# Kernel tuning notes

Hardware: AMD Instinct MI355X
Metric: run time of the kernel (lower is better)

The kernel has to match this reference:

```python
import jax, jax.numpy as jnp
import numpy as np

D_MODEL = 2048
NUM_HEADS = 16
HEAD_DIM = D_MODEL // NUM_HEADS  # 128
BASE = 10000.0


def rotate_half(x):
    x1, x2 = x[..., : x.shape[-1] // 2], x[..., x.shape[-1] // 2 :]
    return jnp.concatenate((-x2, x1), axis=-1)


def setup_inputs() -> dict:
    key = jax.random.key(0)
    ks = jax.random.split(key, 9)
    B, S, D = 2, 2048, D_MODEL
    s = 1.0 / np.sqrt(D)
    return {
        "x": jax.random.normal(ks[0], (B, S, D), dtype=jnp.float32),
        "Wq": jax.random.normal(ks[1], (D, D), dtype=jnp.float32) * s,
        "bq": jnp.zeros((D,), dtype=jnp.float32),
        "Wk": jax.random.normal(ks[2], (D, D), dtype=jnp.float32) * s,
        "bk": jnp.zeros((D,), dtype=jnp.float32),
        "Wv": jax.random.normal(ks[3], (D, D), dtype=jnp.float32) * s,
        "bv": jnp.zeros((D,), dtype=jnp.float32),
        "Wo": jax.random.normal(ks[4], (D, D), dtype=jnp.float32) * s,
        "bo": jnp.zeros((D,), dtype=jnp.float32),
    }


def reference(x, Wq, bq, Wk, bk, Wv, bv, Wo, bo):
    B, S, D = x.shape
    H, hd = NUM_HEADS, HEAD_DIM

    def proj(W, b):
        # nn.Linear: x @ W^T + b, then split heads -> [B, H, S, hd]
        return (x @ W.T + b).reshape(B, S, H, hd).transpose(0, 2, 1, 3)

    q = proj(Wq, bq)
    k = proj(Wk, bk)
    v = proj(Wv, bv)

    # Rotary embedding table (note: original applies cos()/sin() to a
    # tensor that already contains [sin(si), cos(si)] — reproduced faithfully).
    positions = jnp.arange(S, dtype=jnp.float32)
    inv_freq = 1.0 / (BASE ** (jnp.arange(0, hd, 2, dtype=jnp.float32) / hd))
    sinusoid = positions[:, None] * inv_freq[None, :]            # [S, hd/2]
    emb = jnp.concatenate((jnp.sin(sinusoid), jnp.cos(sinusoid)), axis=-1)  # [S, hd]
    cos_e = jnp.cos(emb)  # broadcast over [B, H, S, hd]
    sin_e = jnp.sin(emb)

    q_rot = q * cos_e + rotate_half(q) * sin_e
    k_rot = k * cos_e + rotate_half(k) * sin_e

    scale = 1.0 / jnp.sqrt(jnp.asarray(hd, dtype=x.dtype))
    attn = jnp.einsum("bhqd,bhkd->bhqk", q_rot, k_rot) * scale
    attn = jax.nn.softmax(attn, axis=-1)
    out = jnp.einsum("bhqk,bhkd->bhqd", attn, v)
    out = out.transpose(0, 2, 1, 3).reshape(B, S, D)
    return out @ Wo.T + bo
```

## Files before the change

kernel.cpp:

```cpp
#include <hip/hip_runtime.h>
#include <math.h>

#define D_MODEL 2048
#define NHEADS  16
#define HD      128
#define SEQ     2048
#define BATCH   2
#define SCALE   0.08838834764831845f
#define SMAX    20.0f

typedef __attribute__((ext_vector_type(8))) short short8;
typedef __attribute__((ext_vector_type(4))) float f32x4;

#define MFMA16(a,b,c) __builtin_amdgcn_mfma_f32_16x16x32_bf16((a),(b),(c),0,0,0)

__device__ __forceinline__ unsigned short f2bf(float x){
    unsigned u = __float_as_uint(x);
    return (unsigned short)((u + 0x7FFFu + ((u>>16)&1u)) >> 16);
}
__device__ __forceinline__ float bf2f(unsigned short h){ return __uint_as_float(((unsigned)h)<<16); }

__device__ __forceinline__ void async16(void* lds, const void* g){
    __builtin_amdgcn_global_load_lds((const __attribute__((address_space(1))) unsigned int*)g,
                                     (__attribute__((address_space(3))) unsigned int*)lds, 16, 0, 0);
}

__device__ __forceinline__ void split4(float4 v, ushort4* h, ushort4* l){
    h->x=f2bf(v.x); l->x=f2bf(v.x-bf2f(h->x));
    h->y=f2bf(v.y); l->y=f2bf(v.y-bf2f(h->y));
    h->z=f2bf(v.z); l->z=f2bf(v.z-bf2f(h->z));
    h->w=f2bf(v.w); l->w=f2bf(v.w-bf2f(h->w));
}

__global__ __launch_bounds__(256)
void prep_all(const float* __restrict__ x, const float* __restrict__ Wq,
              const float* __restrict__ Wk, const float* __restrict__ Wv,
              unsigned short* __restrict__ Xhi, unsigned short* __restrict__ Xlo,
              unsigned short* __restrict__ WqHi, unsigned short* __restrict__ WqLo,
              unsigned short* __restrict__ WkHi, unsigned short* __restrict__ WkLo,
              unsigned short* __restrict__ WvHi,
              float4* __restrict__ tab)
{
    const int b = blockIdx.x, t = threadIdx.x;
    if (b < 8192) {
        int i = b*256 + t;
        ushort4 h,l; split4(((const float4*)x)[i], &h, &l);
        ((ushort4*)Xhi)[i]=h; ((ushort4*)Xlo)[i]=l;
    } else if (b < 12288) {
        int i = (b-8192)*256 + t;
        ushort4 h,l; split4(((const float4*)Wq)[i], &h, &l);
        ((ushort4*)WqHi)[i]=h; ((ushort4*)WqLo)[i]=l;
    } else if (b < 16384) {
        int i = (b-12288)*256 + t;
        ushort4 h,l; split4(((const float4*)Wk)[i], &h, &l);
        ((ushort4*)WkHi)[i]=h; ((ushort4*)WkLo)[i]=l;
    } else if (b < 20480) {
        int i = (b-16384)*256 + t;
        ushort4 h,l; split4(((const float4*)Wv)[i], &h, &l);
        ((ushort4*)WvHi)[i]=h;
    } else {
        int i = (b-20480)*256 + t;
        int s = i >> 6, d = i & 63;
        float f = powf(10000.0f, -(float)d * (1.0f/64.0f));
        float sv = (float)s * f;
        float sn = sinf(sv), cs = cosf(sv);
        tab[i] = (float4){cosf(sn), sinf(sn), cosf(cs), sinf(cs)};
    }
}

__global__ __launch_bounds__(256)
void split_w(const float* __restrict__ src, unsigned short* __restrict__ hi,
             unsigned short* __restrict__ lo, int n4)
{
    int i = blockIdx.x*256 + threadIdx.x;
    if (i >= n4) return;
    ushort4 h,l; split4(((const float4*)src)[i], &h, &l);
    ((ushort4*)hi)[i]=h; ((ushort4*)lo)[i]=l;
}

__global__ __launch_bounds__(256,2)
void gemm_qkv(const unsigned short* __restrict__ Xhi_g, const unsigned short* __restrict__ Xlo_g,
              const unsigned short* __restrict__ wsplit,
              const float* __restrict__ bq, const float* __restrict__ bk, const float* __restrict__ bv,
              const float4* __restrict__ tab,
              unsigned short* __restrict__ Qhi, unsigned short* __restrict__ Qlo,
              unsigned short* __restrict__ Khi, unsigned short* __restrict__ Klo,
              unsigned short* __restrict__ Vt)
{
    const int z = blockIdx.z;
    const unsigned short* Whi = wsplit + (size_t)z*8388608u;
    const unsigned short* Wlo = Whi + 4194304u;
    const float* bias = (z==0)?bq:((z==1)?bk:bv);

    const int t = threadIdx.x, w = t>>6, lane = t&63;
    const int quad = lane>>4, l15 = lane&15;
    const int mhalf = (w>>1)*64, nhalf = (w&1)*64;
    const int m0 = blockIdx.y*128, n0 = blockIdx.x*128;

    __shared__ __align__(16) unsigned short gsm[17408];
    unsigned short* Ahi = gsm;
    unsigned short* Alo = gsm + 4096;
    unsigned short* Bhi = gsm + 8192;
    unsigned short* Blo = gsm + 12288;

    f32x4 acc[4][4];
#pragma unroll
    for (int i=0;i<4;i++)
#pragma unroll
        for (int j=0;j<4;j++) acc[i][j] = (f32x4){0.f,0.f,0.f,0.f};

    for (int kt=0; kt<2048; kt+=32) {
        __syncthreads();
#pragma unroll
        for (int j=0;j<2;j++){
            int idx=t+256*j; int rw=idx>>2, sg=idx&3;
            int sgp = sg ^ ((rw>>1)&3);
            size_t goffA = (size_t)(m0+rw)*2048 + kt + sgp*8;
            size_t goffB = (size_t)(n0+rw)*2048 + kt + sgp*8;
            async16((char*)&Ahi[rw*32+sg*8], Xhi_g + goffA);
            async16((char*)&Alo[rw*32+sg*8], Xlo_g + goffA);
            async16((char*)&Bhi[rw*32+sg*8], Whi + goffB);
            if (z != 2)
                async16((char*)&Blo[rw*32+sg*8], Wlo + goffB);
        }
        __syncthreads();

        short8 af_h[4], af_l[4], bf_h[4], bf_l[4];
#pragma unroll
        for (int mi=0;mi<4;mi++){
            int m = mhalf + mi*16 + l15;
            int c = (quad ^ ((m>>1)&3))*8;
            af_h[mi] = *(const short8*)&Ahi[m*32 + c];
            af_l[mi] = *(const short8*)&Alo[m*32 + c];
        }
#pragma unroll
        for (int ni=0;ni<4;ni++){
            int n = nhalf + ni*16 + l15;
            int c = (quad ^ ((n>>1)&3))*8;
            bf_h[ni] = *(const short8*)&Bhi[n*32 + c];
            if (z != 2) bf_l[ni] = *(const short8*)&Blo[n*32 + c];
        }
#pragma unroll
        for (int mi=0;mi<4;mi++)
#pragma unroll
            for (int ni=0;ni<4;ni++){
                acc[mi][ni] = MFMA16(af_h[mi], bf_h[ni], acc[mi][ni]);
                acc[mi][ni] = MFMA16(af_l[mi], bf_h[ni], acc[mi][ni]);
                if (z != 2) acc[mi][ni] = MFMA16(af_h[mi], bf_l[ni], acc[mi][ni]);
            }
    }
    __syncthreads();

#pragma unroll
    for (int ni=0;ni<4;ni++){
        float bv_ = bias[n0 + nhalf + ni*16 + l15];
#pragma unroll
        for (int mi=0;mi<4;mi++){
            acc[mi][ni][0]+=bv_; acc[mi][ni][1]+=bv_; acc[mi][ni][2]+=bv_; acc[mi][ni][3]+=bv_;
        }
    }

    const int h = blockIdx.x;
    if (z == 2) {
#pragma unroll
        for (int mi=0;mi<4;mi++)
#pragma unroll
        for (int ni=0;ni<4;ni++)
#pragma unroll
        for (int r=0;r<4;r++){
            int d = nhalf + ni*16 + l15;
            int ml = mhalf + mi*16 + quad*4 + r;
            gsm[d*136 + ml] = f2bf(acc[mi][ni][r]);
        }
        __syncthreads();
        const int b = m0>>11, s0 = m0&2047;
        unsigned short* vdst = Vt + ((size_t)(b*16+h)*128)*2048;
        const int dr = t>>1, half = (t&1)*64;
#pragma unroll
        for (int j=0;j<8;j++){
            uint4 v = *(const uint4*)&gsm[dr*136 + half + j*8];
            *(uint4*)(vdst + (size_t)dr*2048 + s0 + half + j*8) = v;
        }
    } else {
        float* xch = (float*)gsm;
        unsigned short* OHi = (z==0)?Qhi:Khi;
        unsigned short* OLo = (z==0)?Qlo:Klo;
        const float scl = (z==0)?SCALE:1.0f;
        const int b = m0>>11;
        const size_t bhbase = ((size_t)(b*16+h)*2048);

        if (!(w & 1)) {
#pragma unroll
            for (int mi=0;mi<4;mi++)
#pragma unroll
            for (int ni=2;ni<4;ni++)
#pragma unroll
            for (int r=0;r<4;r++)
                xch[(mhalf+mi*16+quad*4+r)*68 + (ni-2)*16+l15] = acc[mi][ni][r];
        } else {
#pragma unroll
            for (int mi=0;mi<4;mi++)
#pragma unroll
            for (int ni=0;ni<2;ni++)
#pragma unroll
            for (int r=0;r<4;r++)
                xch[(mhalf+mi*16+quad*4+r)*68 + 32 + ni*16+l15] = acc[mi][ni][r];
        }
        __syncthreads();

        if (!(w & 1)) {
#pragma unroll
            for (int ni2=0;ni2<2;ni2++){
                int d = ni2*16 + l15;
#pragma unroll
                for (int mi=0;mi<4;mi++)
#pragma unroll
                for (int r=0;r<4;r++){
                    int ml = mhalf + mi*16 + quad*4 + r;
                    int s = (m0 + ml) & 2047;
                    float4 tv = tab[s*64 + d];
                    float c_lo = acc[mi][ni2][r];
                    float c_hi = xch[ml*68 + 32 + d];
                    float o1 = (c_lo*tv.x - c_hi*tv.y)*scl;
                    float o2 = (c_hi*tv.z + c_lo*tv.w)*scl;
                    size_t base = (bhbase + s)*128;
                    unsigned short h1=f2bf(o1); OHi[base+d]=h1;    OLo[base+d]=f2bf(o1-bf2f(h1));
                    unsigned short h2=f2bf(o2); OHi[base+64+d]=h2; OLo[base+64+d]=f2bf(o2-bf2f(h2));
                }
            }
        } else {
#pragma unroll
            for (int ni2=0;ni2<2;ni2++){
                int d = 32 + ni2*16 + l15;
#pragma unroll
                for (int mi=0;mi<4;mi++)
#pragma unroll
                for (int r=0;r<4;r++){
                    int ml = mhalf + mi*16 + quad*4 + r;
                    int s = (m0 + ml) & 2047;
                    float4 tv = tab[s*64 + d];
                    float c_lo = xch[ml*68 + (d-32)];
                    float c_hi = acc[mi][ni2+2][r];
                    float o1 = (c_lo*tv.x - c_hi*tv.y)*scl;
                    float o2 = (c_hi*tv.z + c_lo*tv.w)*scl;
                    size_t base = (bhbase + s)*128;
                    unsigned short h1=f2bf(o1); OHi[base+d]=h1;    OLo[base+d]=f2bf(o1-bf2f(h1));
                    unsigned short h2=f2bf(o2); OHi[base+64+d]=h2; OLo[base+64+d]=f2bf(o2-bf2f(h2));
                }
            }
        }
    }
}

__global__ __launch_bounds__(256,2)
void flash_mfma(const unsigned short* __restrict__ Qhi, const unsigned short* __restrict__ Qlo,
                const unsigned short* __restrict__ Khi, const unsigned short* __restrict__ Klo,
                const unsigned short* __restrict__ Vt,
                unsigned short* __restrict__ Ohi, unsigned short* __restrict__ Olo)
{
    const int t=threadIdx.x, w=t>>6, lane=t&63, quad=lane>>4, l15=lane&15;
    const int bh = blockIdx.y, qt = blockIdx.x;

    __shared__ __align__(16) unsigned short sm[32768];
    unsigned short* Ps = sm + 24576 + w*2048;

    short8 qf[2][2][4];
    const size_t qrow = (size_t)bh*2048 + qt*128 + w*32;
#pragma unroll
    for (int mb=0;mb<2;mb++){
        size_t r = qrow + mb*16 + l15;
#pragma unroll
        for (int kc=0;kc<4;kc++){
            qf[0][mb][kc] = *(const short8*)(Qhi + r*128 + kc*32 + quad*8);
            qf[1][mb][kc] = *(const short8*)(Qlo + r*128 + kc*32 + quad*8);
        }
    }

    f32x4 O[2][8];
#pragma unroll
    for (int mb=0;mb<2;mb++)
#pragma unroll
        for (int nb=0;nb<8;nb++) O[mb][nb]=(f32x4){0.f,0.f,0.f,0.f};
    float lrow[2][4];
#pragma unroll
    for (int mb=0;mb<2;mb++)
#pragma unroll
        for (int r=0;r<4;r++) lrow[mb][r]=0.f;

    const char* KhiB = (const char*)(Khi + (size_t)bh*2048*128);
    const char* KloB = (const char*)(Klo + (size_t)bh*2048*128);
    const unsigned short* VtB = Vt + (size_t)bh*128*2048;
    char* smb = (char*)sm;

    for (int kt=0; kt<2048; kt+=64) {
#pragma unroll
        for (int i=0;i<4;i++){
            int o16 = t + 256*i;
            int krow = o16>>4, kc = o16&15;
            int kcp = kc ^ (krow&15);
            async16(smb + i*4096 + t*16,         KhiB + (size_t)kt*256 + krow*256 + kcp*16);
            async16(smb + 16384 + i*4096 + t*16, KloB + (size_t)kt*256 + krow*256 + kcp*16);
            int d = (t>>3) + i*32, c = t&7;
            int cp = c ^ (d&7);
            async16(smb + 32768 + i*4096 + t*16, VtB + (size_t)d*2048 + kt + cp*8);
        }
        __syncthreads();

        f32x4 S[2][4];
#pragma unroll
        for (int mb=0;mb<2;mb++)
#pragma unroll
            for (int nb=0;nb<4;nb++) S[mb][nb]=(f32x4){0.f,0.f,0.f,0.f};
#pragma unroll
        for (int kc=0;kc<4;kc++)
#pragma unroll
        for (int nb=0;nb<4;nb++){
            int m = nb*16+l15;
            int c = ((kc*4+quad) ^ (m&15))*8;
            short8 kh = *(const short8*)&sm[m*128 + c];
            short8 kl = *(const short8*)&sm[8192 + m*128 + c];
#pragma unroll
            for (int mb=0;mb<2;mb++){
                S[mb][nb] = MFMA16(qf[0][mb][kc], kh, S[mb][nb]);
                S[mb][nb] = MFMA16(qf[1][mb][kc], kh, S[mb][nb]);
                S[mb][nb] = MFMA16(qf[0][mb][kc], kl, S[mb][nb]);
            }
        }

#pragma unroll
        for (int mb=0;mb<2;mb++)
#pragma unroll
        for (int nb=0;nb<4;nb++)
#pragma unroll
        for (int r=0;r<4;r++){
            float p = __expf(S[mb][nb][r] - SMAX);
            lrow[mb][r] += p;
            int q = mb*16 + quad*4 + r;
            int c = nb*16 + l15;
            Ps[q*64 + (((c>>3)^(q&7))<<3) + (c&7)] = f2bf(p);
        }

#pragma unroll
        for (int kc2=0;kc2<2;kc2++){
            short8 pf0 = *(const short8*)&Ps[(l15)*64      + (((kc2*4+quad)^(l15&7))<<3)];
            short8 pf1 = *(const short8*)&Ps[(16+l15)*64   + (((kc2*4+quad)^(l15&7))<<3)];
#pragma unroll
            for (int nb=0;nb<8;nb++){
                int d = nb*16+l15;
                int c = ((kc2*4+quad) ^ (d&7))*8;
                short8 vf = *(const short8*)&sm[16384 + d*64 + c];
                O[0][nb] = MFMA16(pf0, vf, O[0][nb]);
                O[1][nb] = MFMA16(pf1, vf, O[1][nb]);
            }
        }
        __syncthreads();
    }

#pragma unroll
    for (int mb=0;mb<2;mb++)
#pragma unroll
        for (int d=1;d<16;d<<=1)
#pragma unroll
            for (int r=0;r<4;r++) lrow[mb][r] += __shfl_xor(lrow[mb][r], d);

    const int b = bh>>4, h = bh&15;
#pragma unroll
    for (int mb=0;mb<2;mb++)
#pragma unroll
    for (int nb=0;nb<8;nb++)
#pragma unroll
    for (int r=0;r<4;r++){
        float v = O[mb][nb][r] / lrow[mb][r];
        int qg = qt*128 + w*32 + mb*16 + quad*4 + r;
        size_t base = ((size_t)(b*2048 + qg))*2048 + h*128 + nb*16 + l15;
        unsigned short hh = f2bf(v);
        Ohi[base]=hh; Olo[base]=f2bf(v-bf2f(hh));
    }
}

__global__ __launch_bounds__(256,2)
void gemm_out(const unsigned short* __restrict__ Ahi_g, const unsigned short* __restrict__ Alo_g,
              const unsigned short* __restrict__ Whi_g, const unsigned short* __restrict__ Wlo_g,
              const float* __restrict__ bias, float* __restrict__ out)
{
    const int t = threadIdx.x, w = t>>6, lane = t&63;
    const int quad = lane>>4, l15 = lane&15;
    const int mhalf = (w>>1)*64, nhalf = (w&1)*64;
    const int m0 = blockIdx.y*128, n0 = blockIdx.x*128;

    __shared__ __align__(16) unsigned short gsm[16384];
    unsigned short* Ahi = gsm;
    unsigned short* Alo = gsm + 4096;
    unsigned short* Bhi = gsm + 8192;
    unsigned short* Blo = gsm + 12288;

    f32x4 acc[4][4];
#pragma unroll
    for (int i=0;i<4;i++)
#pragma unroll
        for (int j=0;j<4;j++) acc[i][j] = (f32x4){0.f,0.f,0.f,0.f};

    for (int kt=0; kt<2048; kt+=32) {
        __syncthreads();
#pragma unroll
        for (int j=0;j<2;j++){
            int idx=t+256*j; int rw=idx>>2, sg=idx&3;
            int sgp = sg ^ ((rw>>1)&3);
            async16((char*)&Ahi[rw*32+sg*8], Ahi_g + (size_t)(m0+rw)*2048 + kt + sgp*8);
            async16((char*)&Alo[rw*32+sg*8], Alo_g + (size_t)(m0+rw)*2048 + kt + sgp*8);
            async16((char*)&Bhi[rw*32+sg*8], Whi_g + (size_t)(n0+rw)*2048 + kt + sgp*8);
            async16((char*)&Blo[rw*32+sg*8], Wlo_g + (size_t)(n0+rw)*2048 + kt + sgp*8);
        }
        __syncthreads();

        short8 af_h[4], af_l[4], bf_h[4], bf_l[4];
#pragma unroll
        for (int mi=0;mi<4;mi++){
            int m = mhalf + mi*16 + l15;
            int c = (quad ^ ((m>>1)&3))*8;
            af_h[mi] = *(const short8*)&Ahi[m*32 + c];
            af_l[mi] = *(const short8*)&Alo[m*32 + c];
        }
#pragma unroll
        for (int ni=0;ni<4;ni++){
            int n = nhalf + ni*16 + l15;
            int c = (quad ^ ((n>>1)&3))*8;
            bf_h[ni] = *(const short8*)&Bhi[n*32 + c];
            bf_l[ni] = *(const short8*)&Blo[n*32 + c];
        }
#pragma unroll
        for (int mi=0;mi<4;mi++)
#pragma unroll
            for (int ni=0;ni<4;ni++){
                acc[mi][ni] = MFMA16(af_h[mi], bf_h[ni], acc[mi][ni]);
                acc[mi][ni] = MFMA16(af_l[mi], bf_h[ni], acc[mi][ni]);
                acc[mi][ni] = MFMA16(af_h[mi], bf_l[ni], acc[mi][ni]);
            }
    }

#pragma unroll
    for (int ni=0;ni<4;ni++){
        int n = n0 + nhalf + ni*16 + l15;
        float bv_ = bias[n];
#pragma unroll
        for (int mi=0;mi<4;mi++)
#pragma unroll
        for (int r=0;r<4;r++){
            int m = m0 + mhalf + mi*16 + quad*4 + r;
            out[(size_t)m*2048 + n] = acc[mi][ni][r] + bv_;
        }
    }
}

extern "C" void kernel_launch(void* const* d_in, const int* in_sizes, int n_in,
                              void* d_out, int out_size, void* d_ws, size_t ws_size,
                              hipStream_t stream)
{
    (void)in_sizes; (void)n_in; (void)out_size; (void)ws_size;
    const float* x  = (const float*)d_in[0];
    const float* Wq = (const float*)d_in[1];
    const float* bq = (const float*)d_in[2];
    const float* Wk = (const float*)d_in[3];
    const float* bk = (const float*)d_in[4];
    const float* Wv = (const float*)d_in[5];
    const float* bv = (const float*)d_in[6];
    const float* Wo = (const float*)d_in[7];
    const float* bo = (const float*)d_in[8];
    float* out = (float*)d_out;

    unsigned short* wsB = (unsigned short*)d_ws;
    unsigned short* C0  = wsB + 20971520u;
    unsigned short* Qhi = C0;
    unsigned short* Qlo = C0 + 8388608u;
    unsigned short* Khi = C0 + 16777216u;
    unsigned short* Klo = C0 + 25165824u;
    unsigned short* Vt  = C0 + 33554432u;
    float4* tab = (float4*)(wsB + 62914560u);

    unsigned short* Xhi = (unsigned short*)d_out;
    unsigned short* Xlo = Xhi + 8388608u;

    prep_all<<<20992,256,0,stream>>>(x, Wq, Wk, Wv,
                                     Xhi, Xlo,
                                     wsB,            wsB+4194304u,
                                     wsB+8388608u,   wsB+12582912u,
                                     wsB+16777216u,  tab);

    gemm_qkv<<<dim3(16,32,3),256,0,stream>>>(Xhi, Xlo, wsB, bq,bk,bv, tab,
                                             Qhi,Qlo,Khi,Klo,Vt);

    unsigned short* Ohi = wsB;
    unsigned short* Olo = wsB + 8388608u;
    flash_mfma<<<dim3(16,32),256,0,stream>>>(Qhi,Qlo,Khi,Klo,Vt, Ohi, Olo);

    unsigned short* WoHi = C0;
    unsigned short* WoLo = C0 + 4194304u;
    split_w<<<4096,256,0,stream>>>(Wo, WoHi, WoLo, 1048576);

    gemm_out<<<dim3(16,32),256,0,stream>>>(Ohi, Olo, WoHi, WoLo, bo, out);
}
```

Measured before the change: 662.0 us.

## Triple-buffer GEMM core with async LDS prefetch and larger 256x128 tiles

Replaces the synchronous load-then-compute GEMM loops with a shared gemm_core that triple-buffers A/B tiles in dynamic LDS. It prefetches two k-steps ahead using vmcnt waits and interleaves the staging loads with MFMA phases under s_setprio. Blocks grow to 512 threads with 256x128 tiles, and the QKV kernel is split into separate Q/K and V kernels so the V path skips the lo-weight loads. This is meant to hide global load latency and cut barrier stalls, at the cost of 144KB LDS per block, which lowers occupancy.

```diff
diff --git a/kernel.cpp b/kernel.cpp
--- a/kernel.cpp
+++ b/kernel.cpp
@@ -78,30 +78,129 @@
     ((ushort4*)hi)[i]=h; ((ushort4*)lo)[i]=l;
 }
 
-__global__ __launch_bounds__(256,2)
-void gemm_qkv(const unsigned short* __restrict__ Xhi_g, const unsigned short* __restrict__ Xlo_g,
-              const unsigned short* __restrict__ wsplit,
-              const float* __restrict__ bq, const float* __restrict__ bk, const float* __restrict__ bv,
-              const float4* __restrict__ tab,
-              unsigned short* __restrict__ Qhi, unsigned short* __restrict__ Qlo,
-              unsigned short* __restrict__ Khi, unsigned short* __restrict__ Klo,
-              unsigned short* __restrict__ Vt)
-{
+template<bool THREE, int Q>
+__device__ __forceinline__ void phase_mfma(const unsigned short* Bh, const unsigned short* Bl,
+                                           const short8 (&ah)[4], const short8 (&al)[4],
+                                           f32x4 (&acc)[4][4], int wn, int quad, int l15)
+{
+    int n = wn*64 + Q*16 + l15;
+    int c = (quad ^ ((n>>1)&3))*8;
+    short8 bh_ = *(const short8*)&Bh[n*32 + c];
+    short8 bl_ = {};
+    if constexpr (THREE) bl_ = *(const short8*)&Bl[n*32 + c];
+    __builtin_amdgcn_s_setprio(1);
+    acc[0][Q] = MFMA16(ah[0], bh_, acc[0][Q]);
+    acc[1][Q] = MFMA16(ah[1], bh_, acc[1][Q]);
+    acc[2][Q] = MFMA16(ah[2], bh_, acc[2][Q]);
+    acc[3][Q] = MFMA16(ah[3], bh_, acc[3][Q]);
+    acc[0][Q] = MFMA16(al[0], bh_, acc[0][Q]);
+    acc[1][Q] = MFMA16(al[1], bh_, acc[1][Q]);
+    acc[2][Q] = MFMA16(al[2], bh_, acc[2][Q]);
+    acc[3][Q] = MFMA16(al[3], bh_, acc[3][Q]);
+    if constexpr (THREE) {
+        acc[0][Q] = MFMA16(ah[0], bl_, acc[0][Q]);
+        acc[1][Q] = MFMA16(ah[1], bl_, acc[1][Q]);
+        acc[2][Q] = MFMA16(ah[2], bl_, acc[2][Q]);
+        acc[3][Q] = MFMA16(ah[3], bl_, acc[3][Q]);
+    }
+    __builtin_amdgcn_s_setprio(0);
+}
+
+template<bool THREE>
+__device__ __forceinline__ void gemm_core(const unsigned short* __restrict__ Agh,
+                                          const unsigned short* __restrict__ Agl,
+                                          const unsigned short* __restrict__ Bgh,
+                                          const unsigned short* __restrict__ Bgl,
+                                          unsigned short* lds, int m0, int n0,
+                                          f32x4 (&acc)[4][4])
+{
+    const int t = threadIdx.x, w = t>>6, lane = t&63;
+    const int quad = lane>>4, l15 = lane&15;
+    const int wm = w>>1, wn = w&1;
+
+    unsigned short *c0 = lds, *c1 = lds + 24576, *c2 = lds + 49152;
+
+    auto stageA = [&](unsigned short* P, const unsigned short* SRC, int u, int kt2){
+        int idx = t + u*512; int rw = idx>>2, sg = idx&3;
+        int sgp = sg ^ ((rw>>1)&3);
+        async16((char*)(P + rw*32 + sg*8), SRC + (size_t)(m0+rw)*2048 + kt2 + sgp*8);
+    };
+    auto stageB = [&](unsigned short* P, const unsigned short* SRC, int kt2){
+        int rw = t>>2, sg = t&3; int sgp = sg ^ ((rw>>1)&3);
+        async16((char*)(P + rw*32 + sg*8), SRC + (size_t)(n0+rw)*2048 + kt2 + sgp*8);
+    };
+
+    stageA(c0,        Agh, 0, 0);  stageA(c0,        Agh, 1, 0);
+    stageA(c0+8192,   Agl, 0, 0);  stageA(c0+8192,   Agl, 1, 0);
+    stageB(c0+16384,  Bgh, 0);
+    if constexpr (THREE) stageB(c0+20480, Bgl, 0);
+    stageA(c1,        Agh, 0, 32); stageA(c1,        Agh, 1, 32);
+    stageA(c1+8192,   Agl, 0, 32); stageA(c1+8192,   Agl, 1, 32);
+    stageB(c1+16384,  Bgh, 32);
+    if constexpr (THREE) stageB(c1+20480, Bgl, 32);
+
+    for (int kt = 0; kt < 64; ++kt) {
+        if (kt == 63) {
+            asm volatile("s_waitcnt vmcnt(0)" ::: "memory");
+        } else if constexpr (THREE) {
+            asm volatile("s_waitcnt vmcnt(6)" ::: "memory");
+        } else {
+            asm volatile("s_waitcnt vmcnt(5)" ::: "memory");
+        }
+        __builtin_amdgcn_s_barrier();
+        __builtin_amdgcn_sched_barrier(0);
+
+        const unsigned short* Ah = c0;
+        const unsigned short* Al = c0 + 8192;
+        const unsigned short* Bh = c0 + 16384;
+        const unsigned short* Bl = c0 + 20480;
+        const int  kt2 = (kt+2)*32;
+        const bool st  = (kt < 62);
+
+        short8 ah[4], al[4];
+#pragma unroll
+        for (int mi=0;mi<4;mi++){
+            int m = wm*64 + mi*16 + l15;
+            int c = (quad ^ ((m>>1)&3))*8;
+            ah[mi] = *(const short8*)&Ah[m*32 + c];
+            al[mi] = *(const short8*)&Al[m*32 + c];
+        }
+        if (st){ stageA(c2,       Agh, 0, kt2); stageA(c2,       Agh, 1, kt2); }
+        phase_mfma<THREE,0>(Bh, Bl, ah, al, acc, wn, quad, l15);
+        __builtin_amdgcn_s_barrier();
+
+        if (st){ stageA(c2+8192,  Agl, 0, kt2); stageA(c2+8192,  Agl, 1, kt2); }
+        phase_mfma<THREE,1>(Bh, Bl, ah, al, acc, wn, quad, l15);
+        __builtin_amdgcn_s_barrier();
+
+        if (st){ stageB(c2+16384, Bgh, kt2); }
+        phase_mfma<THREE,2>(Bh, Bl, ah, al, acc, wn, quad, l15);
+        __builtin_amdgcn_s_barrier();
+
+        if constexpr (THREE) { if (st) stageB(c2+20480, Bgl, kt2); }
+        phase_mfma<THREE,3>(Bh, Bl, ah, al, acc, wn, quad, l15);
+        __builtin_amdgcn_s_barrier();
+
+        unsigned short* tmp = c0; c0 = c1; c1 = c2; c2 = tmp;
+    }
+}
+
+__global__ __launch_bounds__(512,2)
+void gemm_qk(const unsigned short* __restrict__ Xhi_g, const unsigned short* __restrict__ Xlo_g,
+             const unsigned short* __restrict__ wsplit,
+             const float* __restrict__ bq, const float* __restrict__ bk,
+             const float4* __restrict__ tab,
+             unsigned short* __restrict__ Qhi, unsigned short* __restrict__ Qlo,
+             unsigned short* __restrict__ Khi, unsigned short* __restrict__ Klo)
+{
+    extern __shared__ unsigned short ldsm[];
     const int z = blockIdx.z;
     const unsigned short* Whi = wsplit + (size_t)z*8388608u;
     const unsigned short* Wlo = Whi + 4194304u;
-    const float* bias = (z==0)?bq:((z==1)?bk:bv);
-
     const int t = threadIdx.x, w = t>>6, lane = t&63;
     const int quad = lane>>4, l15 = lane&15;
-    const int mhalf = (w>>1)*64, nhalf = (w&1)*64;
-    const int m0 = blockIdx.y*128, n0 = blockIdx.x*128;
-
-    __shared__ __align__(16) unsigned short gsm[17408];
-    unsigned short* Ahi = gsm;
-    unsigned short* Alo = gsm + 4096;
-    unsigned short* Bhi = gsm + 8192;
-    unsigned short* Blo = gsm + 12288;
+    const int wm = w>>1, wn = w&1;
+    const int m0 = blockIdx.y*256, n0 = blockIdx.x*128;
 
     f32x4 acc[4][4];
 #pragma unroll
@@ -109,145 +208,170 @@
 #pragma unroll
         for (int j=0;j<4;j++) acc[i][j] = (f32x4){0.f,0.f,0.f,0.f};
 
-    for (int kt=0; kt<2048; kt+=32) {
-        __syncthreads();
-#pragma unroll
-        for (int j=0;j<2;j++){
-            int idx=t+256*j; int rw=idx>>2, sg=idx&3;
-            int sgp = sg ^ ((rw>>1)&3);
-            size_t goffA = (size_t)(m0+rw)*2048 + kt + sgp*8;
-            size_t goffB = (size_t)(n0+rw)*2048 + kt + sgp*8;
-            async16((char*)&Ahi[rw*32+sg*8], Xhi_g + goffA);
-            async16((char*)&Alo[rw*32+sg*8], Xlo_g + goffA);
-            async16((char*)&Bhi[rw*32+sg*8], Whi + goffB);
-            if (z != 2)
-                async16((char*)&Blo[rw*32+sg*8], Wlo + goffB);
-        }
-        __syncthreads();
-
-        short8 af_h[4], af_l[4], bf_h[4], bf_l[4];
-#pragma unroll
-        for (int mi=0;mi<4;mi++){
-            int m = mhalf + mi*16 + l15;
-            int c = (quad ^ ((m>>1)&3))*8;
-            af_h[mi] = *(const short8*)&Ahi[m*32 + c];
-            af_l[mi] = *(const short8*)&Alo[m*32 + c];
-        }
-#pragma unroll
-        for (int ni=0;ni<4;ni++){
-            int n = nhalf + ni*16 + l15;
-            int c = (quad ^ ((n>>1)&3))*8;
-            bf_h[ni] = *(const short8*)&Bhi[n*32 + c];
-            if (z != 2) bf_l[ni] = *(const short8*)&Blo[n*32 + c];
-        }
-#pragma unroll
-        for (int mi=0;mi<4;mi++)
-#pragma unroll
-            for (int ni=0;ni<4;ni++){
-                acc[mi][ni] = MFMA16(af_h[mi], bf_h[ni], acc[mi][ni]);
-                acc[mi][ni] = MFMA16(af_l[mi], bf_h[ni], acc[mi][ni]);
-                if (z != 2) acc[mi][ni] = MFMA16(af_h[mi], bf_l[ni], acc[mi][ni]);
-            }
-    }
+    gemm_core<true>(Xhi_g, Xlo_g, Whi, Wlo, ldsm, m0, n0, acc);
     __syncthreads();
 
+    const float* bias = (z==0)?bq:bk;
 #pragma unroll
     for (int ni=0;ni<4;ni++){
-        float bv_ = bias[n0 + nhalf + ni*16 + l15];
+        float bv_ = bias[n0 + wn*64 + ni*16 + l15];
 #pragma unroll
         for (int mi=0;mi<4;mi++){
             acc[mi][ni][0]+=bv_; acc[mi][ni][1]+=bv_; acc[mi][ni][2]+=bv_; acc[mi][ni][3]+=bv_;
         }
     }
 
+    float* xch = (float*)ldsm;
+    unsigned short* OHi = (z==0)?Qhi:Khi;
+    unsigned short* OLo = (z==0)?Qlo:Klo;
+    const float scl = (z==0)?SCALE:1.0f;
     const int h = blockIdx.x;
-    if (z == 2) {
+    const int b = m0>>11;
+    const size_t bhbase = ((size_t)(b*16+h)*2048);
+
+    if (wn == 0) {
 #pragma unroll
         for (int mi=0;mi<4;mi++)
 #pragma unroll
-        for (int ni=0;ni<4;ni++)
+        for (int ni=2;ni<4;ni++)
+#pragma unroll
+        for (int r=0;r<4;r++)
+            xch[(wm*64+mi*16+quad*4+r)*68 + (ni-2)*16+l15] = acc[mi][ni][r];
+    } else {
+#pragma unroll
+        for (int mi=0;mi<4;mi++)
+#pragma unroll
+        for (int ni=0;ni<2;ni++)
+#pragma unroll
+        for (int r=0;r<4;r++)
+            xch[(wm*64+mi*16+quad*4+r)*68 + 32 + ni*16+l15] = acc[mi][ni][r];
+    }
+    __syncthreads();
+
+    if (wn == 0) {
+#pragma unroll
+        for (int ni2=0;ni2<2;ni2++){
+            int d = ni2*16 + l15;
+#pragma unroll
+            for (int mi=0;mi<4;mi++)
+#pragma unroll
+            for (int r=0;r<4;r++){
+                int ml = wm*64 + mi*16 + quad*4 + r;
+                int s = (m0 + ml) & 2047;
+                float4 tv = tab[s*64 + d];
+                float c_lo = acc[mi][ni2][r];
+                float c_hi = xch[ml*68 + 32 + d];
+                float o1 = (c_lo*tv.x - c_hi*tv.y)*scl;
+                float o2 = (c_hi*tv.z + c_lo*tv.w)*scl;
+                size_t base = (bhbase + s)*128;
+                unsigned short h1=f2bf(o1); OHi[base+d]=h1;    OLo[base+d]=f2bf(o1-bf2f(h1));
+                unsigned short h2=f2bf(o2); OHi[base+64+d]=h2; OLo[base+64+d]=f2bf(o2-bf2f(h2));
+            }
+        }
+    } else {
+#pragma unroll
+        for (int ni2=0;ni2<2;ni2++){
+            int d = 32 + ni2*16 + l15;
+#pragma unroll
+            for (int mi=0;mi<4;mi++)
+#pragma unroll
+            for (int r=0;r<4;r++){
+                int ml = wm*64 + mi*16 + quad*4 + r;
+                int s = (m0 + ml) & 2047;
+                float4 tv = tab[s*64 + d];
+                float c_lo = xch[ml*68 + (d-32)];
+                float c_hi = acc[mi][ni2+2][r];
+                float o1 = (c_lo*tv.x - c_hi*tv.y)*scl;
+                float o2 = (c_hi*tv.z + c_lo*tv.w)*scl;
+                size_t base = (bhbase + s)*128;
+                unsigned short h1=f2bf(o1); OHi[base+d]=h1;    OLo[base+d]=f2bf(o1-bf2f(h1));
+                unsigned short h2=f2bf(o2); OHi[base+64+d]=h2; OLo[base+64+d]=f2bf(o2-bf2f(h2));
+            }
+        }
+    }
+}
+
+__global__ __launch_bounds__(512,2)
+void gemm_v(const unsigned short* __restrict__ Xhi_g, const unsigned short* __restrict__ Xlo_g,
+            const unsigned short* __restrict__ WvHi,
+            const float* __restrict__ bv, unsigned short* __restrict__ Vt)
+{
+    extern __shared__ unsigned short ldsm[];
+    const int t = threadIdx.x, w = t>>6, lane = t&63;
+    const int quad = lane>>4, l15 = lane&15;
+    const int wm = w>>1, wn = w&1;
+    const int m0 = blockIdx.y*256, n0 = blockIdx.x*128;
+
+    f32x4 acc[4][4];
+#pragma unroll
+    for (int i=0;i<4;i++)
+#pragma unroll
+        for (int j=0;j<4;j++) acc[i][j] = (f32x4){0.f,0.f,0.f,0.f};
+
+    gemm_core<false>(Xhi_g, Xlo_g, WvHi, nullptr, ldsm, m0, n0, acc);
+    __syncthreads();
+
+#pragma unroll
+    for (int ni=0;ni<4;ni++){
+        float bv_ = bv[n0 + wn*64 + ni*16 + l15];
+#pragma unroll
+        for (int mi=0;mi<4;mi++){
+            acc[mi][ni][0]+=bv_; acc[mi][ni][1]+=bv_; acc[mi][ni][2]+=bv_; acc[mi][ni][3]+=bv_;
+        }
+    }
+
+    unsigned short* vb = ldsm;
+#pragma unroll
+    for (int mi=0;mi<4;mi++)
+#pragma unroll
+    for (int ni=0;ni<4;ni++)
+#pragma unroll
+    for (int r=0;r<4;r++){
+        int d  = wn*64 + ni*16 + l15;
+        int ml = wm*64 + mi*16 + quad*4 + r;
+        vb[d*264 + ml] = f2bf(acc[mi][ni][r]);
+    }
+    __syncthreads();
+
+    const int b = m0>>11, s0 = m0&2047, h = blockIdx.x;
+    unsigned short* vdst = Vt + (size_t)(b*16+h)*128*2048;
+    const int dr = t>>2, part = (t&3)*64;
+#pragma unroll
+    for (int j=0;j<8;j++){
+        uint4 v = *(const uint4*)&vb[dr*264 + part + j*8];
+        *(uint4*)(vdst + (size_t)dr*2048 + s0 + part + j*8) = v;
+    }
+}
+
+__global__ __launch_bounds__(512,2)
+void gemm_o(const unsigned short* __restrict__ Ahi_g, const unsigned short* __restrict__ Alo_g,
+            const unsigned short* __restrict__ Whi_g, const unsigned short* __restrict__ Wlo_g,
+            const float* __restrict__ bias, float* __restrict__ out)
+{
+    extern __shared__ unsigned short ldsm[];
+    const int t = threadIdx.x, w = t>>6, lane = t&63;
+    const int quad = lane>>4, l15 = lane&15;
+    const int wm = w>>1, wn = w&1;
+    const int m0 = blockIdx.y*256, n0 = blockIdx.x*128;
+
+    f32x4 acc[4][4];
+#pragma unroll
+    for (int i=0;i<4;i++)
+#pragma unroll
+        for (int j=0;j<4;j++) acc[i][j] = (f32x4){0.f,0.f,0.f,0.f};
+
+    gemm_core<true>(Ahi_g, Alo_g, Whi_g, Wlo_g, ldsm, m0, n0, acc);
+
+#pragma unroll
+    for (int ni=0;ni<4;ni++){
+        int n = n0 + wn*64 + ni*16 + l15;
+        float bv_ = bias[n];
+#pragma unroll
+        for (int mi=0;mi<4;mi++)
 #pragma unroll
         for (int r=0;r<4;r++){
-            int d = nhalf + ni*16 + l15;
-            int ml = mhalf + mi*16 + quad*4 + r;
-            gsm[d*136 + ml] = f2bf(acc[mi][ni][r]);
-        }
-        __syncthreads();
-        const int b = m0>>11, s0 = m0&2047;
-        unsigned short* vdst = Vt + ((size_t)(b*16+h)*128)*2048;
-        const int dr = t>>1, half = (t&1)*64;
-#pragma unroll
-        for (int j=0;j<8;j++){
-            uint4 v = *(const uint4*)&gsm[dr*136 + half + j*8];
-            *(uint4*)(vdst + (size_t)dr*2048 + s0 + half + j*8) = v;
-        }
-    } else {
-        float* xch = (float*)gsm;
-        unsigned short* OHi = (z==0)?Qhi:Khi;
-        unsigned short* OLo = (z==0)?Qlo:Klo;
-        const float scl = (z==0)?SCALE:1.0f;
-        const int b = m0>>11;
-        const size_t bhbase = ((size_t)(b*16+h)*2048);
-
-        if (!(w & 1)) {
-#pragma unroll
-            for (int mi=0;mi<4;mi++)
-#pragma unroll
-            for (int ni=2;ni<4;ni++)
-#pragma unroll
-            for (int r=0;r<4;r++)
-                xch[(mhalf+mi*16+quad*4+r)*68 + (ni-2)*16+l15] = acc[mi][ni][r];
-        } else {
-#pragma unroll
-            for (int mi=0;mi<4;mi++)
-#pragma unroll
-            for (int ni=0;ni<2;ni++)
-#pragma unroll
-            for (int r=0;r<4;r++)
-                xch[(mhalf+mi*16+quad*4+r)*68 + 32 + ni*16+l15] = acc[mi][ni][r];
-        }
-        __syncthreads();
-
-        if (!(w & 1)) {
-#pragma unroll
-            for (int ni2=0;ni2<2;ni2++){
-                int d = ni2*16 + l15;
-#pragma unroll
-                for (int mi=0;mi<4;mi++)
-#pragma unroll
-                for (int r=0;r<4;r++){
-                    int ml = mhalf + mi*16 + quad*4 + r;
-                    int s = (m0 + ml) & 2047;
-                    float4 tv = tab[s*64 + d];
-                    float c_lo = acc[mi][ni2][r];
-                    float c_hi = xch[ml*68 + 32 + d];
-                    float o1 = (c_lo*tv.x - c_hi*tv.y)*scl;
-                    float o2 = (c_hi*tv.z + c_lo*tv.w)*scl;
-                    size_t base = (bhbase + s)*128;
-                    unsigned short h1=f2bf(o1); OHi[base+d]=h1;    OLo[base+d]=f2bf(o1-bf2f(h1));
-                    unsigned short h2=f2bf(o2); OHi[base+64+d]=h2; OLo[base+64+d]=f2bf(o2-bf2f(h2));
-                }
-            }
-        } else {
-#pragma unroll
-            for (int ni2=0;ni2<2;ni2++){
-                int d = 32 + ni2*16 + l15;
-#pragma unroll
-                for (int mi=0;mi<4;mi++)
-#pragma unroll
-                for (int r=0;r<4;r++){
-                    int ml = mhalf + mi*16 + quad*4 + r;
-                    int s = (m0 + ml) & 2047;
-                    float4 tv = tab[s*64 + d];
-                    float c_lo = xch[ml*68 + (d-32)];
-                    float c_hi = acc[mi][ni2+2][r];
-                    float o1 = (c_lo*tv.x - c_hi*tv.y)*scl;
-                    float o2 = (c_hi*tv.z + c_lo*tv.w)*scl;
-                    size_t base = (bhbase + s)*128;
-                    unsigned short h1=f2bf(o1); OHi[base+d]=h1;    OLo[base+d]=f2bf(o1-bf2f(h1));
-                    unsigned short h2=f2bf(o2); OHi[base+64+d]=h2; OLo[base+64+d]=f2bf(o2-bf2f(h2));
-                }
-            }
+            int m = m0 + wm*64 + mi*16 + quad*4 + r;
+            out[(size_t)m*2048 + n] = acc[mi][ni][r] + bv_;
         }
     }
 }
@@ -375,80 +499,6 @@
         size_t base = ((size_t)(b*2048 + qg))*2048 + h*128 + nb*16 + l15;
         unsigned short hh = f2bf(v);
         Ohi[base]=hh; Olo[base]=f2bf(v-bf2f(hh));
-    }
-}
-
-__global__ __launch_bounds__(256,2)
-void gemm_out(const unsigned short* __restrict__ Ahi_g, const unsigned short* __restrict__ Alo_g,
-              const unsigned short* __restrict__ Whi_g, const unsigned short* __restrict__ Wlo_g,
-              const float* __restrict__ bias, float* __restrict__ out)
-{
-    const int t = threadIdx.x, w = t>>6, lane = t&63;
-    const int quad = lane>>4, l15 = lane&15;
-    const int mhalf = (w>>1)*64, nhalf = (w&1)*64;
-    const int m0 = blockIdx.y*128, n0 = blockIdx.x*128;
-
-    __shared__ __align__(16) unsigned short gsm[16384];
-    unsigned short* Ahi = gsm;
-    unsigned short* Alo = gsm + 4096;
-    unsigned short* Bhi = gsm + 8192;
-    unsigned short* Blo = gsm + 12288;
-
-    f32x4 acc[4][4];
-#pragma unroll
-    for (int i=0;i<4;i++)
-#pragma unroll
-        for (int j=0;j<4;j++) acc[i][j] = (f32x4){0.f,0.f,0.f,0.f};
-
-    for (int kt=0; kt<2048; kt+=32) {
-        __syncthreads();
-#pragma unroll
-        for (int j=0;j<2;j++){
-            int idx=t+256*j; int rw=idx>>2, sg=idx&3;
-            int sgp = sg ^ ((rw>>1)&3);
-            async16((char*)&Ahi[rw*32+sg*8], Ahi_g + (size_t)(m0+rw)*2048 + kt + sgp*8);
-            async16((char*)&Alo[rw*32+sg*8], Alo_g + (size_t)(m0+rw)*2048 + kt + sgp*8);
-            async16((char*)&Bhi[rw*32+sg*8], Whi_g + (size_t)(n0+rw)*2048 + kt + sgp*8);
-            async16((char*)&Blo[rw*32+sg*8], Wlo_g + (size_t)(n0+rw)*2048 + kt + sgp*8);
-        }
-        __syncthreads();
-
-        short8 af_h[4], af_l[4], bf_h[4], bf_l[4];
-#pragma unroll
-        for (int mi=0;mi<4;mi++){
-            int m = mhalf + mi*16 + l15;
-            int c = (quad ^ ((m>>1)&3))*8;
-            af_h[mi] = *(const short8*)&Ahi[m*32 + c];
-            af_l[mi] = *(const short8*)&Alo[m*32 + c];
-        }
-#pragma unroll
-        for (int ni=0;ni<4;ni++){
-            int n = nhalf + ni*16 + l15;
-            int c = (quad ^ ((n>>1)&3))*8;
-            bf_h[ni] = *(const short8*)&Bhi[n*32 + c];
-            bf_l[ni] = *(const short8*)&Blo[n*32 + c];
-        }
-#pragma unroll
-        for (int mi=0;mi<4;mi++)
-#pragma unroll
-            for (int ni=0;ni<4;ni++){
-                acc[mi][ni] = MFMA16(af_h[mi], bf_h[ni], acc[mi][ni]);
-                acc[mi][ni] = MFMA16(af_l[mi], bf_h[ni], acc[mi][ni]);
-                acc[mi][ni] = MFMA16(af_h[mi], bf_l[ni], acc[mi][ni]);
-            }
-    }
-
-#pragma unroll
-    for (int ni=0;ni<4;ni++){
-        int n = n0 + nhalf + ni*16 + l15;
-        float bv_ = bias[n];
-#pragma unroll
-        for (int mi=0;mi<4;mi++)
-#pragma unroll
-        for (int r=0;r<4;r++){
-            int m = m0 + mhalf + mi*16 + quad*4 + r;
-            out[(size_t)m*2048 + n] = acc[mi][ni][r] + bv_;
-        }
     }
 }
 
@@ -480,14 +530,26 @@
     unsigned short* Xhi = (unsigned short*)d_out;
     unsigned short* Xlo = Xhi + 8388608u;
 
+    static bool attr_done = false;
+    if (!attr_done) {
+        (void)hipFuncSetAttribute(reinterpret_cast<const void*>(&gemm_qk),
+                                  hipFuncAttributeMaxDynamicSharedMemorySize, 147456);
+        (void)hipFuncSetAttribute(reinterpret_cast<const void*>(&gemm_v),
+                                  hipFuncAttributeMaxDynamicSharedMemorySize, 147456);
+        (void)hipFuncSetAttribute(reinterpret_cast<const void*>(&gemm_o),
+                                  hipFuncAttributeMaxDynamicSharedMemorySize, 147456);
+        attr_done = true;
+    }
+
     prep_all<<<20992,256,0,stream>>>(x, Wq, Wk, Wv,
                                      Xhi, Xlo,
                                      wsB,            wsB+4194304u,
                                      wsB+8388608u,   wsB+12582912u,
                                      wsB+16777216u,  tab);
 
-    gemm_qkv<<<dim3(16,32,3),256,0,stream>>>(Xhi, Xlo, wsB, bq,bk,bv, tab,
-                                             Qhi,Qlo,Khi,Klo,Vt);
+    gemm_qk<<<dim3(16,16,2),512,147456,stream>>>(Xhi, Xlo, wsB, bq, bk, tab,
+                                                 Qhi, Qlo, Khi, Klo);
+    gemm_v <<<dim3(16,16),  512,147456,stream>>>(Xhi, Xlo, wsB+16777216u, bv, Vt);
 
     unsigned short* Ohi = wsB;
     unsigned short* Olo = wsB + 8388608u;
@@ -497,5 +559,5 @@
     unsigned short* WoLo = C0 + 4194304u;
     split_w<<<4096,256,0,stream>>>(Wo, WoHi, WoLo, 1048576);
 
-    gemm_out<<<dim3(16,32),256,0,stream>>>(Ohi, Olo, WoHi, WoLo, bo, out);
-}
+    gemm_o<<<dim3(16,16),512,147456,stream>>>(Ohi, Olo, WoHi, WoLo, bo, out);
+}
```

New measurement: 632.3 us. 1.05x faster.
